# Kernel optimization log

Measured on AMD Instinct MI355X. Metric: run time of the kernel, lower is better.

Reference implementation:

```python
import jax, jax.numpy as jnp
import numpy as np

B, C, H, W = 8, 256, 128, 128
RED = 4
LAMBDA_C = 0.5
LAMBDA_S = 0.5
EPS = 1e-5  # BatchNorm eps (eval mode: running stats)


def setup_inputs() -> dict:
    key = jax.random.key(0)
    ks = jax.random.split(key, 8)
    Cr = C // RED
    x1 = jax.random.normal(ks[0], (B, C, H, W), jnp.float32)
    x2 = jax.random.normal(ks[1], (B, C, H, W), jnp.float32)
    # feature_extractor: 1x1 conv (dim*2 -> dim), kaiming-ish scale
    w_fe = jax.random.normal(ks[2], (C, 2 * C), jnp.float32) * (2.0 / (2 * C)) ** 0.5
    bn_gamma = jnp.ones((C,), jnp.float32)
    bn_beta = jnp.zeros((C,), jnp.float32)
    bn_mean = jnp.zeros((C,), jnp.float32)
    bn_var = jnp.ones((C,), jnp.float32)
    # conv_weight_generator: C -> C//r -> 9C (1x1 convs on pooled vector)
    w_cg1 = jax.random.normal(ks[3], (Cr, C), jnp.float32) * (2.0 / C) ** 0.5
    w_cg2 = jax.random.normal(ks[4], (9 * C, Cr), jnp.float32) * (2.0 / Cr) ** 0.5
    # attention_generator: C -> C//r -> 2
    w_ag1 = jax.random.normal(ks[5], (Cr, C), jnp.float32) * (2.0 / C) ** 0.5
    w_ag2 = jax.random.normal(ks[6], (2, Cr), jnp.float32) * (2.0 / Cr) ** 0.5
    return {"x1": x1, "x2": x2, "w_fe": w_fe, "bn_gamma": bn_gamma,
            "bn_beta": bn_beta, "bn_mean": bn_mean, "bn_var": bn_var,
            "w_cg1": w_cg1, "w_cg2": w_cg2, "w_ag1": w_ag1, "w_ag2": w_ag2}


def reference(x1, x2, w_fe, bn_gamma, bn_beta, bn_mean, bn_var,
              w_cg1, w_cg2, w_ag1, w_ag2):
    Bv, Cv, Hv, Wv = x1.shape
    # feature_extractor: 1x1 conv + BN (eval) + ReLU
    cat = jnp.concatenate([x1, x2], axis=1)                       # [B,2C,H,W]
    s = jnp.einsum('oi,bihw->bohw', w_fe, cat)                    # [B,C,H,W]
    scale = (bn_gamma / jnp.sqrt(bn_var + EPS))[None, :, None, None]
    shift = (bn_beta - bn_mean * bn_gamma / jnp.sqrt(bn_var + EPS))[None, :, None, None]
    s = jax.nn.relu(s * scale + shift)
    # global average pool -> per-sample vectors
    pooled = s.mean(axis=(2, 3))                                  # [B,C]
    # dynamic per-sample, per-channel 3x3 kernels
    hcg = jax.nn.relu(pooled @ w_cg1.T)                           # [B,C//r]
    cw = (hcg @ w_cg2.T).reshape(Bv * Cv, 1, 3, 3)                # [B*C,1,3,3]
    # attention scalars (2 per sample)
    attn = jax.nn.sigmoid(jax.nn.relu(pooled @ w_ag1.T) @ w_ag2.T)  # [B,2]

    def dyn_conv(x):
        xr = x.reshape(1, Bv * Cv, Hv, Wv)
        y = jax.lax.conv_general_dilated(
            xr, cw, window_strides=(1, 1), padding='SAME',
            feature_group_count=Bv * Cv,
            dimension_numbers=('NCHW', 'OIHW', 'NCHW'))
        return y.reshape(Bv, Cv, Hv, Wv)

    d1 = dyn_conv(x1)
    d2 = dyn_conv(x2)
    a1 = attn[:, 0][:, None, None, None]
    a2 = attn[:, 1][:, None, None, None]
    out_x1 = x1 + LAMBDA_C * a1 * d1
    out_x2 = x2 + LAMBDA_C * a2 * d2
    return LAMBDA_S * out_x1 + (1.0 - LAMBDA_S) * out_x2
```

## Files before the change

kernel.cpp:

```cpp
#include <hip/hip_runtime.h>
#include <stdint.h>
#include <math.h>

#define HW_ 16384
#define C_  256
#define NT  8

typedef short bf16x8 __attribute__((ext_vector_type(8)));
typedef float f32x4  __attribute__((ext_vector_type(4)));
typedef unsigned int u32;

__device__ __forceinline__ unsigned short f2bf(float f) {
  union { float f; unsigned u; } v; v.f = f;
  unsigned u = v.u;
  u += 0x7fffu + ((u >> 16) & 1u);
  return (unsigned short)(u >> 16);
}

__global__ __launch_bounds__(256) void k0_prep(
    const float* __restrict__ w_fe, const float* __restrict__ gamma,
    const float* __restrict__ beta, const float* __restrict__ mean,
    const float* __restrict__ var, unsigned short* __restrict__ Wp,
    float* __restrict__ scale, float* __restrict__ shift)
{
  int i = blockIdx.x * 256 + threadIdx.x;
  if (i < 131072) {
    int e  = i & 7;
    int r  = (i >> 3) & 15;
    int mf = (i >> 7) & 15;
    int kg = (i >> 11) & 3;
    int ks = i >> 13;
    int row = mf * 16 + r;
    int k   = ks * 32 + kg * 8 + e;
    Wp[i] = f2bf(w_fe[row * 512 + k]);
  }
  if (i < 256) {
    float sc = gamma[i] * rsqrtf(var[i] + 1e-5f);
    scale[i] = sc;
    shift[i] = beta[i] - mean[i] * sc;
  }
}

__global__ __launch_bounds__(1024, 4) void k1_gemm_pool(
    const float* __restrict__ x1, const float* __restrict__ x2,
    const unsigned short* __restrict__ Wp,
    const float* __restrict__ scale, const float* __restrict__ shift,
    float* __restrict__ pool_part)
{
  __shared__ __align__(16) char Bl[2][65536];

  const int tid  = threadIdx.x;
  const int wave = tid >> 6;
  const int lane = tid & 63;
  const int r15  = lane & 15;
  const int kg   = lane >> 4;
  const int blk  = blockIdx.x;
  const int b    = blk >> 5;
  const int tile0 = (blk & 31) * NT;

  const float* xb1 = x1 + (size_t)b * C_ * HW_;
  const float* xb2 = x2 + (size_t)b * C_ * HW_;

  const int v  = tid & 7;
  const int u2 = ((tid >> 3) & 7) * 2;
  const int kp = wave * 8 + v;

  const int WBASE = (kp >> 4) * 4096 + ((kp >> 2) & 3) * 256 + (kp & 3) * 4
                    + u2 * 16;

  bf16x8 Af[16];
#pragma unroll
  for (int ks = 0; ks < 16; ++ks)
    Af[ks] = *(const bf16x8*)(Wp + ks * 8192 + kg * 2048 + wave * 128 + r15 * 8);

  const int chbase = wave * 16 + kg * 4;
  const float4 sc4 = *(const float4*)&scale[chbase];
  const float4 sh4 = *(const float4*)&shift[chbase];

  float pool0 = 0.f, pool1 = 0.f, pool2 = 0.f, pool3 = 0.f;

  float2 gRA[4], gRB[4];

#define ISSUE_H(H, P0)                                                        \
  {                                                                           \
    const float* s0 = ((H) == 0 ? xb1 : xb2) + (size_t)(kp * 2) * HW_         \
                      + (P0) + u2;                                            \
    _Pragma("unroll")                                                         \
    for (int G = 0; G < 4; ++G) {                                             \
      gRA[G] = *(const float2*)(s0 + G * 16);                                 \
      gRB[G] = *(const float2*)(s0 + G * 16 + HW_);                           \
    }                                                                         \
  }

#define WRITE_H(H, BUF)                                                       \
  {                                                                           \
    char* wb = (char*)(BUF) + WBASE + (H) * 32768;                            \
    _Pragma("unroll")                                                         \
    for (int G = 0; G < 4; ++G) {                                             \
      u32 w0 = (u32)f2bf(gRA[G].x) | ((u32)f2bf(gRB[G].x) << 16);             \
      u32 w1 = (u32)f2bf(gRA[G].y) | ((u32)f2bf(gRB[G].y) << 16);             \
      *(u32*)(wb + G * 1024) = w0;                                            \
      *(u32*)(wb + G * 1024 + 16) = w1;                                       \
    }                                                                         \
  }

#define COMPUTE_H(H, BUF)                                                     \
  {                                                                           \
    _Pragma("unroll")                                                         \
    for (int ks8 = 0; ks8 < 8; ++ks8) {                                       \
      const int ks = (H) * 8 + ks8;                                           \
      const char* rbase = (const char*)(BUF) + ks * 4096 + lane * 16;         \
      _Pragma("unroll")                                                       \
      for (int nf = 0; nf < 4; ++nf) {                                        \
        bf16x8 bfr = *(const bf16x8*)(rbase + nf * 1024);                     \
        acc[nf] = __builtin_amdgcn_mfma_f32_16x16x32_bf16(Af[ks], bfr,        \
                                                          acc[nf], 0, 0, 0); \
      }                                                                       \
    }                                                                         \
  }

  ISSUE_H(0, tile0 * 64) WRITE_H(0, Bl[0])
  ISSUE_H(1, tile0 * 64) WRITE_H(1, Bl[0])
  __syncthreads();

  for (int tt = 0; tt < NT; ++tt) {
    f32x4 acc[4];
#pragma unroll
    for (int nf = 0; nf < 4; ++nf) acc[nf] = (f32x4){0.f, 0.f, 0.f, 0.f};

    const int p0n = (tile0 + tt + 1) * 64;
    const bool more = (tt + 1 < NT);
    const char* cb = Bl[tt & 1];
    char* nxt = Bl[(tt + 1) & 1];

    if (more) ISSUE_H(0, p0n)
    COMPUTE_H(0, cb)
    if (more) { WRITE_H(0, nxt) ISSUE_H(1, p0n) }
    COMPUTE_H(1, cb)
    if (more) WRITE_H(1, nxt)

#pragma unroll
    for (int nf = 0; nf < 4; ++nf) {
      pool0 += fmaxf(acc[nf][0] * sc4.x + sh4.x, 0.f);
      pool1 += fmaxf(acc[nf][1] * sc4.y + sh4.y, 0.f);
      pool2 += fmaxf(acc[nf][2] * sc4.z + sh4.z, 0.f);
      pool3 += fmaxf(acc[nf][3] * sc4.w + sh4.w, 0.f);
    }
    __syncthreads();
  }

#pragma unroll
  for (int m = 1; m < 16; m <<= 1) {
    pool0 += __shfl_xor(pool0, m);
    pool1 += __shfl_xor(pool1, m);
    pool2 += __shfl_xor(pool2, m);
    pool3 += __shfl_xor(pool3, m);
  }
  if (r15 == 0) {
    float* dst = pool_part + (size_t)blk * 256 + chbase;
    dst[0] = pool0; dst[1] = pool1; dst[2] = pool2; dst[3] = pool3;
  }
}

__global__ __launch_bounds__(256) void k2_small(
    const float* __restrict__ pool_part,
    const float* __restrict__ w_cg1, const float* __restrict__ w_cg2,
    const float* __restrict__ w_ag1, const float* __restrict__ w_ag2,
    float* __restrict__ cw, float* __restrict__ coef)
{
  __shared__ float pl[256];
  __shared__ float hl[64];
  const int bi = blockIdx.x;
  const int b = bi / 10, j = bi % 10;
  const int t = threadIdx.x;
  float s = 0.f;
  const float* base = pool_part + (size_t)b * 32 * 256 + t;
  for (int blk = 0; blk < 32; ++blk) s += base[blk * 256];
  pl[t] = s * (1.0f / 16384.0f);
  __syncthreads();
  if (j < 9) {
    if (t < 64) {
      float h = 0.f;
      for (int i = 0; i < 256; ++i) h += pl[i] * w_cg1[t * 256 + i];
      hl[t] = fmaxf(h, 0.f);
    }
    __syncthreads();
    const int o = t * 9 + j;
    float acc = 0.f;
    for (int jj = 0; jj < 64; ++jj) acc += hl[jj] * w_cg2[o * 64 + jj];
    cw[b * 2304 + o] = acc;
  } else {
    if (t < 64) {
      float a = 0.f;
      for (int i = 0; i < 256; ++i) a += pl[i] * w_ag1[t * 256 + i];
      hl[t] = fmaxf(a, 0.f);
    }
    __syncthreads();
    if (t < 2) {
      float acc = 0.f;
      for (int jj = 0; jj < 64; ++jj) acc += hl[jj] * w_ag2[t * 64 + jj];
      coef[b * 2 + t] = 0.25f / (1.0f + expf(-acc));
    }
  }
}

__global__ __launch_bounds__(256) void k3_dynconv(
    const float* __restrict__ x1, const float* __restrict__ x2,
    const float* __restrict__ cw, const float* __restrict__ coef,
    float* __restrict__ out)
{
  __shared__ float t1[34 * 128];
  __shared__ float t2[34 * 128];
  const int tid   = threadIdx.x;
  const int blk   = blockIdx.x;
  const int strip = blk & 3;
  const int c     = (blk >> 2) & 255;
  const int b     = blk >> 10;
  const int h0    = strip * 32;

  const size_t plane = ((size_t)b * C_ + c) * HW_;
  const float* p1 = x1 + plane;
  const float* p2 = x2 + plane;

  float tp[9];
#pragma unroll
  for (int e = 0; e < 9; ++e) tp[e] = cw[(b * C_ + c) * 9 + e];
  const float c1 = coef[b * 2 + 0];
  const float c2 = coef[b * 2 + 1];

  for (int f = tid; f < 1088; f += 256) {
    int row = f >> 5;
    int c4  = (f & 31) << 2;
    int gh  = h0 - 1 + row;
    float4 v1 = make_float4(0.f, 0.f, 0.f, 0.f), v2 = v1;
    if (gh >= 0 && gh < 128) {
      v1 = *(const float4*)&p1[gh * 128 + c4];
      v2 = *(const float4*)&p2[gh * 128 + c4];
    }
    *(float4*)&t1[row * 128 + c4] = v1;
    *(float4*)&t2[row * 128 + c4] = v2;
  }
  __syncthreads();

  for (int i = 0; i < 16; ++i) {
    int q   = tid + i * 256;
    int r   = q >> 7;
    int col = q & 127;
    int lr  = r + 1;
    const bool lok = col > 0, rok = col < 127;
    float d1 = 0.f, d2 = 0.f;
#pragma unroll
    for (int dy = 0; dy < 3; ++dy) {
      const float* row1 = &t1[(lr - 1 + dy) * 128];
      const float* row2 = &t2[(lr - 1 + dy) * 128];
      float a1v = lok ? row1[col - 1] : 0.f;
      float b1v = row1[col];
      float e1v = rok ? row1[col + 1] : 0.f;
      float a2v = lok ? row2[col - 1] : 0.f;
      float b2v = row2[col];
      float e2v = rok ? row2[col + 1] : 0.f;
      d1 += a1v * tp[dy * 3 + 0] + b1v * tp[dy * 3 + 1] + e1v * tp[dy * 3 + 2];
      d2 += a2v * tp[dy * 3 + 0] + b2v * tp[dy * 3 + 1] + e2v * tp[dy * 3 + 2];
    }
    float v1 = t1[lr * 128 + col];
    float v2 = t2[lr * 128 + col];
    out[plane + (size_t)(h0 + r) * 128 + col] = 0.5f * (v1 + v2) + c1 * d1 + c2 * d2;
  }
}

extern "C" void kernel_launch(void* const* d_in, const int* in_sizes, int n_in,
                              void* d_out, int out_size, void* d_ws, size_t ws_size,
                              hipStream_t stream) {
  const float* x1    = (const float*)d_in[0];
  const float* x2    = (const float*)d_in[1];
  const float* w_fe  = (const float*)d_in[2];
  const float* gamma = (const float*)d_in[3];
  const float* beta  = (const float*)d_in[4];
  const float* mean  = (const float*)d_in[5];
  const float* var   = (const float*)d_in[6];
  const float* w_cg1 = (const float*)d_in[7];
  const float* w_cg2 = (const float*)d_in[8];
  const float* w_ag1 = (const float*)d_in[9];
  const float* w_ag2 = (const float*)d_in[10];
  float* out = (float*)d_out;

  char* ws = (char*)d_ws;
  unsigned short* Wp = (unsigned short*)(ws);
  float* scale     = (float*)(ws + 262144);
  float* shift     = (float*)(ws + 263168);
  float* pool_part = (float*)(ws + 264192);
  float* cw        = (float*)(ws + 526336);
  float* coef      = (float*)(ws + 600064);

  k0_prep<<<512, 256, 0, stream>>>(w_fe, gamma, beta, mean, var, Wp, scale, shift);
  k1_gemm_pool<<<256, 1024, 0, stream>>>(x1, x2, Wp, scale, shift, pool_part);
  k2_small<<<80, 256, 0, stream>>>(pool_part, w_cg1, w_cg2, w_ag1, w_ag2, cw, coef);
  k3_dynconv<<<8192, 256, 0, stream>>>(x1, x2, cw, coef, out);
}
```

Baseline: 182.3 us.

## Switch feature-extractor GEMM from bf16 to fp8 MFMA with repacked LDS layout

Converts both the 1x1-conv weights and the activation tiles to fp8 (e4m3) instead of bf16 and uses the 16x16x32 fp8 MFMA. Shared-memory staging buffers halve in size and the global-to-LDS load and write pattern is restructured, so each thread loads 8 channels of 2 pixels and packs them into fp8 words. This cuts LDS footprint, LDS bandwidth and conversion cost in the GEMM+pool kernel. The trade is reduced precision in the pooled features that drive the dynamic kernels, which may hurt accuracy tolerance.

```diff
diff --git a/kernel.cpp b/kernel.cpp
--- a/kernel.cpp
+++ b/kernel.cpp
@@ -6,33 +6,31 @@
 #define C_  256
 #define NT  8
 
-typedef short bf16x8 __attribute__((ext_vector_type(8)));
-typedef float f32x4  __attribute__((ext_vector_type(4)));
+typedef long i64;
+typedef float f32x4 __attribute__((ext_vector_type(4)));
+typedef long i64x2 __attribute__((ext_vector_type(2)));
 typedef unsigned int u32;
-
-__device__ __forceinline__ unsigned short f2bf(float f) {
-  union { float f; unsigned u; } v; v.f = f;
-  unsigned u = v.u;
-  u += 0x7fffu + ((u >> 16) & 1u);
-  return (unsigned short)(u >> 16);
-}
 
 __global__ __launch_bounds__(256) void k0_prep(
     const float* __restrict__ w_fe, const float* __restrict__ gamma,
     const float* __restrict__ beta, const float* __restrict__ mean,
-    const float* __restrict__ var, unsigned short* __restrict__ Wp,
+    const float* __restrict__ var, u32* __restrict__ Wp,
     float* __restrict__ scale, float* __restrict__ shift)
 {
   int i = blockIdx.x * 256 + threadIdx.x;
-  if (i < 131072) {
-    int e  = i & 7;
-    int r  = (i >> 3) & 15;
-    int mf = (i >> 7) & 15;
-    int kg = (i >> 11) & 3;
-    int ks = i >> 13;
-    int row = mf * 16 + r;
-    int k   = ks * 32 + kg * 8 + e;
-    Wp[i] = f2bf(w_fe[row * 512 + k]);
+  if (i < 32768) {
+    int e0  = (i & 1) * 4;
+    int r15 = (i >> 1) & 15;
+    int kg  = (i >> 5) & 3;
+    int mf  = (i >> 7) & 15;
+    int ks  = i >> 11;
+    int row = mf * 16 + r15;
+    int k   = ks * 32 + kg * 8 + e0;
+    const float* src = w_fe + row * 512 + k;
+    u32 w = 0;
+    w = __builtin_amdgcn_cvt_pk_fp8_f32(src[0], src[1], w, false);
+    w = __builtin_amdgcn_cvt_pk_fp8_f32(src[2], src[3], w, true);
+    Wp[i] = w;
   }
   if (i < 256) {
     float sc = gamma[i] * rsqrtf(var[i] + 1e-5f);
@@ -43,11 +41,11 @@
 
 __global__ __launch_bounds__(1024, 4) void k1_gemm_pool(
     const float* __restrict__ x1, const float* __restrict__ x2,
-    const unsigned short* __restrict__ Wp,
+    const u32* __restrict__ Wp,
     const float* __restrict__ scale, const float* __restrict__ shift,
     float* __restrict__ pool_part)
 {
-  __shared__ __align__(16) char Bl[2][65536];
+  __shared__ __align__(16) char Bl[2][32768];
 
   const int tid  = threadIdx.x;
   const int wave = tid >> 6;
@@ -61,17 +59,19 @@
   const float* xb1 = x1 + (size_t)b * C_ * HW_;
   const float* xb2 = x2 + (size_t)b * C_ * HW_;
 
-  const int v  = tid & 7;
-  const int u2 = ((tid >> 3) & 7) * 2;
-  const int kp = wave * 8 + v;
-
-  const int WBASE = (kp >> 4) * 4096 + ((kp >> 2) & 3) * 256 + (kp & 3) * 4
-                    + u2 * 16;
-
-  bf16x8 Af[16];
+  const int p2  = tid & 31;
+  const int k8  = tid >> 5;
+  const int ksL = k8 >> 2;
+  const int kgs = k8 & 3;
+  const int nfs = p2 >> 3;
+  const int L0  = ((2 * p2) & 15) + kgs * 16;
+  const int WB0 = (ksL * 2 + (nfs >> 1)) * 1024 + L0 * 16 + (nfs & 1) * 8;
+
+  i64 Af[16];
 #pragma unroll
   for (int ks = 0; ks < 16; ++ks)
-    Af[ks] = *(const bf16x8*)(Wp + ks * 8192 + kg * 2048 + wave * 128 + r15 * 8);
+    Af[ks] = *(const i64*)((const char*)Wp
+             + ((ks * 16 + wave) * 64 + kg * 16 + r15) * 8);
 
   const int chbase = wave * 16 + kg * 4;
   const float4 sc4 = *(const float4*)&scale[chbase];
@@ -79,29 +79,32 @@
 
   float pool0 = 0.f, pool1 = 0.f, pool2 = 0.f, pool3 = 0.f;
 
-  float2 gRA[4], gRB[4];
+  float2 gR[8];
 
 #define ISSUE_H(H, P0)                                                        \
   {                                                                           \
-    const float* s0 = ((H) == 0 ? xb1 : xb2) + (size_t)(kp * 2) * HW_         \
-                      + (P0) + u2;                                            \
+    const float* s0 = ((H) == 0 ? xb1 : xb2) + (size_t)(k8 * 8) * HW_         \
+                      + (P0) + 2 * p2;                                        \
     _Pragma("unroll")                                                         \
-    for (int G = 0; G < 4; ++G) {                                             \
-      gRA[G] = *(const float2*)(s0 + G * 16);                                 \
-      gRB[G] = *(const float2*)(s0 + G * 16 + HW_);                           \
-    }                                                                         \
+    for (int r = 0; r < 8; ++r) gR[r] = *(const float2*)(s0 + r * HW_);       \
   }
 
 #define WRITE_H(H, BUF)                                                       \
   {                                                                           \
-    char* wb = (char*)(BUF) + WBASE + (H) * 32768;                            \
-    _Pragma("unroll")                                                         \
-    for (int G = 0; G < 4; ++G) {                                             \
-      u32 w0 = (u32)f2bf(gRA[G].x) | ((u32)f2bf(gRB[G].x) << 16);             \
-      u32 w1 = (u32)f2bf(gRA[G].y) | ((u32)f2bf(gRB[G].y) << 16);             \
-      *(u32*)(wb + G * 1024) = w0;                                            \
-      *(u32*)(wb + G * 1024 + 16) = w1;                                       \
-    }                                                                         \
+    u32 a0 = 0, a1 = 0, b0 = 0, b1 = 0;                                       \
+    a0 = __builtin_amdgcn_cvt_pk_fp8_f32(gR[0].x, gR[1].x, a0, false);        \
+    a0 = __builtin_amdgcn_cvt_pk_fp8_f32(gR[2].x, gR[3].x, a0, true);         \
+    a1 = __builtin_amdgcn_cvt_pk_fp8_f32(gR[4].x, gR[5].x, a1, false);        \
+    a1 = __builtin_amdgcn_cvt_pk_fp8_f32(gR[6].x, gR[7].x, a1, true);         \
+    b0 = __builtin_amdgcn_cvt_pk_fp8_f32(gR[0].y, gR[1].y, b0, false);        \
+    b0 = __builtin_amdgcn_cvt_pk_fp8_f32(gR[2].y, gR[3].y, b0, true);         \
+    b1 = __builtin_amdgcn_cvt_pk_fp8_f32(gR[4].y, gR[5].y, b1, false);        \
+    b1 = __builtin_amdgcn_cvt_pk_fp8_f32(gR[6].y, gR[7].y, b1, true);         \
+    char* wb = (char*)(BUF) + WB0 + (H) * 16384;                              \
+    u32* w0 = (u32*)(wb);                                                     \
+    w0[0] = a0; w0[1] = a1;                                    \
+    u32* w1 = (u32*)(wb + 16);                                                \
+    w1[0] = b0; w1[1] = b1;                                    \
   }
 
 #define COMPUTE_H(H, BUF)                                                     \
@@ -109,12 +112,14 @@
     _Pragma("unroll")                                                         \
     for (int ks8 = 0; ks8 < 8; ++ks8) {                                       \
       const int ks = (H) * 8 + ks8;                                           \
-      const char* rbase = (const char*)(BUF) + ks * 4096 + lane * 16;         \
+      const char* rbase = (const char*)(BUF) + ks * 2048 + lane * 16;         \
       _Pragma("unroll")                                                       \
-      for (int nf = 0; nf < 4; ++nf) {                                        \
-        bf16x8 bfr = *(const bf16x8*)(rbase + nf * 1024);                     \
-        acc[nf] = __builtin_amdgcn_mfma_f32_16x16x32_bf16(Af[ks], bfr,        \
-                                                          acc[nf], 0, 0, 0); \
+      for (int np = 0; np < 2; ++np) {                                        \
+        i64x2 bq = *(const i64x2*)(rbase + np * 1024);                        \
+        acc[np * 2] = __builtin_amdgcn_mfma_f32_16x16x32_fp8_fp8(             \
+            Af[ks], bq.x, acc[np * 2], 0, 0, 0);                              \
+        acc[np * 2 + 1] = __builtin_amdgcn_mfma_f32_16x16x32_fp8_fp8(         \
+            Af[ks], bq.y, acc[np * 2 + 1], 0, 0, 0);                          \
       }                                                                       \
     }                                                                         \
   }
@@ -285,14 +290,14 @@
   float* out = (float*)d_out;
 
   char* ws = (char*)d_ws;
-  unsigned short* Wp = (unsigned short*)(ws);
-  float* scale     = (float*)(ws + 262144);
-  float* shift     = (float*)(ws + 263168);
-  float* pool_part = (float*)(ws + 264192);
-  float* cw        = (float*)(ws + 526336);
-  float* coef      = (float*)(ws + 600064);
-
-  k0_prep<<<512, 256, 0, stream>>>(w_fe, gamma, beta, mean, var, Wp, scale, shift);
+  u32* Wp          = (u32*)(ws);
+  float* scale     = (float*)(ws + 131072);
+  float* shift     = (float*)(ws + 132096);
+  float* pool_part = (float*)(ws + 133120);
+  float* cw        = (float*)(ws + 395264);
+  float* coef      = (float*)(ws + 468992);
+
+  k0_prep<<<128, 256, 0, stream>>>(w_fe, gamma, beta, mean, var, Wp, scale, shift);
   k1_gemm_pool<<<256, 1024, 0, stream>>>(x1, x2, Wp, scale, shift, pool_part);
   k2_small<<<80, 256, 0, stream>>>(pool_part, w_cg1, w_cg2, w_ag1, w_ag2, cw, coef);
   k3_dynconv<<<8192, 256, 0, stream>>>(x1, x2, cw, coef, out);
```

New measurement: 153.1 us. 16.0% less time.
